# Kernel tuning notes

Hardware: AMD Instinct MI355X
Metric: run time of the kernel (lower is better)

The kernel has to match this reference:

```python
import math
import jax, jax.numpy as jnp
import numpy as np


def setup_inputs() -> dict:
    key = jax.random.key(0)
    k1, k2, k3 = jax.random.split(key, 3)
    B, T, D = 4, 2048, 2048
    x = jax.random.normal(k1, (B, T, D), dtype=jnp.float32)
    w_qkv = jax.random.normal(k2, (D, 3 * D), dtype=jnp.float32) * 0.02
    w_proj = jax.random.normal(k3, (D, D), dtype=jnp.float32) * 0.02
    b_proj = jnp.zeros((D,), dtype=jnp.float32)
    return {"x": x, "w_qkv": w_qkv, "w_proj": w_proj, "b_proj": b_proj, "n_head": 16}


def reference(x, w_qkv, w_proj, b_proj, n_head):
    B, T, D = x.shape
    N = n_head
    H = D // N
    qkv = x @ w_qkv                       # (B,T,3D)
    q, k, v = jnp.split(qkv, 3, axis=-1)  # each (B,T,D)
    # NOTE: original torch code does .view(B, n_head, T, H) directly on the
    # (B,T,D) tensor (a raw memory reinterpretation, not a head split+transpose).
    q = q.reshape(B, N, T, H)
    k = k.reshape(B, N, T, H)
    v = v.reshape(B, N, T, H)
    # full T x T score matrix, scaled by sqrt(D) (not sqrt(H)) as in the original
    a = jnp.einsum('bnih,bnjh->bnij', q, k) / math.sqrt(D)  # (B,N,T,T)
    a = jax.nn.softmax(a, axis=3)
    # torch.einsum('bntt,bnth->bnth', a, v): repeated 't' in first operand
    # takes the DIAGONAL of the attention matrix, then elementwise-scales v.
    diag = jnp.diagonal(a, axis1=2, axis2=3)  # (B,N,T)
    o = diag[..., None] * v                   # (B,N,T,H)
    o = jnp.transpose(o, (0, 2, 1, 3)).reshape(B, T, D)
    return o @ w_proj + b_proj
```

## Files before the change

kernel.cpp:

```cpp
#include <hip/hip_runtime.h>
#include <hip/hip_bf16.h>

typedef short bf16x8 __attribute__((ext_vector_type(8)));
typedef float f32x4 __attribute__((ext_vector_type(4)));

__device__ __forceinline__ unsigned short f2bf(float f) {
  union { float f; unsigned int u; } x; x.f = f;
  return (unsigned short)((x.u + 0x7fffu + ((x.u >> 16) & 1u)) >> 16);
}
__device__ __forceinline__ float bf2f(unsigned short u) {
  union { unsigned int u; float f; } x; x.u = ((unsigned int)u) << 16;
  return x.f;
}
__device__ __forceinline__ void gload_lds16(const void* g, void* l) {
  __builtin_amdgcn_global_load_lds((const __attribute__((address_space(1))) void*)g,
                                   (__attribute__((address_space(3))) void*)l, 16, 0, 0);
}

__global__ void cast_f32_bf16(const float* __restrict__ src, unsigned short* __restrict__ dst) {
  int i = blockIdx.x * blockDim.x + threadIdx.x;
  float4 v = reinterpret_cast<const float4*>(src)[i];
  ushort4 o;
  o.x = f2bf(v.x); o.y = f2bf(v.y); o.z = f2bf(v.z); o.w = f2bf(v.w);
  reinterpret_cast<ushort4*>(dst)[i] = o;
}

__global__ void transpose_cast(const float* __restrict__ src, unsigned short* __restrict__ dst,
                               int R, int C) {
  __shared__ float tile[32][33];
  int c0 = blockIdx.x * 32, r0 = blockIdx.y * 32;
  int tx = threadIdx.x, ty = threadIdx.y;
#pragma unroll
  for (int i = 0; i < 4; ++i)
    tile[ty + i * 8][tx] = src[(size_t)(r0 + ty + i * 8) * C + (c0 + tx)];
  __syncthreads();
#pragma unroll
  for (int i = 0; i < 4; ++i)
    dst[(size_t)(c0 + ty + i * 8) * R + (r0 + tx)] = f2bf(tile[tx][ty + i * 8]);
}

template <int EPI>
__global__ __launch_bounds__(512, 2)
void gemm256(const unsigned short* __restrict__ A, const unsigned short* __restrict__ Bt,
             unsigned short* __restrict__ Qo, unsigned short* __restrict__ Ko,
             unsigned short* __restrict__ Vo, float* __restrict__ Cf,
             const float* __restrict__ bias, int M, int N, int K) {
  extern __shared__ __align__(16) char lds[];
  const int tid = threadIdx.x;
  const int lane = tid & 63, wid = tid >> 6;
  const int wm = wid >> 2, wn = wid & 3;
  const int fr = lane & 15, fq = lane >> 4;

  const int nbn = N >> 8;
  const int cpx = gridDim.x >> 3;
  const int id = blockIdx.x;
  const int sw = (id & 7) * cpx + (id >> 3);
  const int bm = sw / nbn, bn = sw % nbn;
  const int row0 = bm << 8, col0 = bn << 8;

  const int NT = K >> 6;

  const int srow = tid >> 3;
  const int scol = ((tid & 7) ^ (srow & 7)) << 3;

  auto stage = [&](int j, int slot) {
    if (j < 4 * NT) {
      const int t = j >> 2, ht = j & 3;
      const int isB = (ht == 1 || ht == 2);
      const int h = (ht >= 2) ? 1 : 0;
      const unsigned short* base = isB ? Bt : A;
      const int grow = (isB ? col0 : row0) + h * 128 + srow;
      const unsigned short* src = base + (size_t)grow * K + t * 64 + scol;
      char* l0 = lds + slot * 16384 + tid * 16;
      gload_lds16(src, l0);
      gload_lds16(src + (size_t)64 * K, l0 + 8192);
    } else {
      char* l0 = lds + 7 * 16384 + tid * 16;
      gload_lds16(A + (tid << 3), l0);
      gload_lds16(A + (tid << 3), l0 + 8192);
    }
  };

  f32x4 acc[2][4][2][2] = {};

  stage(0, 0); stage(1, 1); stage(2, 2); stage(3, 3); stage(4, 4);
  asm volatile("s_waitcnt vmcnt(6)" ::: "memory");
  asm volatile("s_barrier" ::: "memory");

  int sA0 = 0, sB0 = 1, sB1 = 2, sA1 = 3, sst = 5;

  for (int k = 0; k < NT; ++k) {
    const int j0 = 4 * k + 5;
    bf16x8 a[4][2], b0[2][2], b1[2][2];

    {
      const char* Ab = lds + sA0 * 16384;
      const char* Bb = lds + sB0 * 16384;
#pragma unroll
      for (int i2 = 0; i2 < 4; ++i2)
#pragma unroll
        for (int ks = 0; ks < 2; ++ks) {
          const int byte = ((((wm * 4 + i2) * 16 + fr) * 128) + ks * 64 + fq * 16) ^ ((fr & 7) << 4);
          a[i2][ks] = *reinterpret_cast<const bf16x8*>(Ab + byte);
        }
#pragma unroll
      for (int j2 = 0; j2 < 2; ++j2)
#pragma unroll
        for (int ks = 0; ks < 2; ++ks) {
          const int byte = ((((wn * 2 + j2) * 16 + fr) * 128) + ks * 64 + fq * 16) ^ ((fr & 7) << 4);
          b0[j2][ks] = *reinterpret_cast<const bf16x8*>(Bb + byte);
        }
      stage(j0 + 0, sst); sst = (sst == 6) ? 0 : sst + 1;
      asm volatile("s_waitcnt vmcnt(6)" ::: "memory");
      asm volatile("s_barrier" ::: "memory");
      __builtin_amdgcn_s_setprio(1);
#pragma unroll
      for (int i2 = 0; i2 < 4; ++i2)
#pragma unroll
        for (int j2 = 0; j2 < 2; ++j2)
#pragma unroll
          for (int ks = 0; ks < 2; ++ks)
            acc[0][i2][0][j2] =
                __builtin_amdgcn_mfma_f32_16x16x32_bf16(a[i2][ks], b0[j2][ks], acc[0][i2][0][j2], 0, 0, 0);
      __builtin_amdgcn_s_setprio(0);
    }

    {
      const char* Bb = lds + sB1 * 16384;
#pragma unroll
      for (int j2 = 0; j2 < 2; ++j2)
#pragma unroll
        for (int ks = 0; ks < 2; ++ks) {
          const int byte = ((((wn * 2 + j2) * 16 + fr) * 128) + ks * 64 + fq * 16) ^ ((fr & 7) << 4);
          b1[j2][ks] = *reinterpret_cast<const bf16x8*>(Bb + byte);
        }
      stage(j0 + 1, sst); sst = (sst == 6) ? 0 : sst + 1;
      asm volatile("s_waitcnt vmcnt(6)" ::: "memory");
      asm volatile("s_barrier" ::: "memory");
      __builtin_amdgcn_s_setprio(1);
#pragma unroll
      for (int i2 = 0; i2 < 4; ++i2)
#pragma unroll
        for (int j2 = 0; j2 < 2; ++j2)
#pragma unroll
          for (int ks = 0; ks < 2; ++ks)
            acc[0][i2][1][j2] =
                __builtin_amdgcn_mfma_f32_16x16x32_bf16(a[i2][ks], b1[j2][ks], acc[0][i2][1][j2], 0, 0, 0);
      __builtin_amdgcn_s_setprio(0);
    }

    {
      const char* Ab = lds + sA1 * 16384;
#pragma unroll
      for (int i2 = 0; i2 < 4; ++i2)
#pragma unroll
        for (int ks = 0; ks < 2; ++ks) {
          const int byte = ((((wm * 4 + i2) * 16 + fr) * 128) + ks * 64 + fq * 16) ^ ((fr & 7) << 4);
          a[i2][ks] = *reinterpret_cast<const bf16x8*>(Ab + byte);
        }
      stage(j0 + 2, sst); sst = (sst == 6) ? 0 : sst + 1;
      asm volatile("s_waitcnt vmcnt(6)" ::: "memory");
      asm volatile("s_barrier" ::: "memory");
      __builtin_amdgcn_s_setprio(1);
#pragma unroll
      for (int i2 = 0; i2 < 4; ++i2)
#pragma unroll
        for (int j2 = 0; j2 < 2; ++j2)
#pragma unroll
          for (int ks = 0; ks < 2; ++ks)
            acc[1][i2][0][j2] =
                __builtin_amdgcn_mfma_f32_16x16x32_bf16(a[i2][ks], b0[j2][ks], acc[1][i2][0][j2], 0, 0, 0);
      __builtin_amdgcn_s_setprio(0);
    }

    {
      stage(j0 + 3, sst); sst = (sst == 6) ? 0 : sst + 1;
      asm volatile("s_waitcnt vmcnt(6)" ::: "memory");
      asm volatile("s_barrier" ::: "memory");
      __builtin_amdgcn_s_setprio(1);
#pragma unroll
      for (int i2 = 0; i2 < 4; ++i2)
#pragma unroll
        for (int j2 = 0; j2 < 2; ++j2)
#pragma unroll
          for (int ks = 0; ks < 2; ++ks)
            acc[1][i2][1][j2] =
                __builtin_amdgcn_mfma_f32_16x16x32_bf16(a[i2][ks], b1[j2][ks], acc[1][i2][1][j2], 0, 0, 0);
      __builtin_amdgcn_s_setprio(0);
    }

    sA0 += 4; if (sA0 >= 7) sA0 -= 7;
    sB0 += 4; if (sB0 >= 7) sB0 -= 7;
    sB1 += 4; if (sB1 >= 7) sB1 -= 7;
    sA1 += 4; if (sA1 >= 7) sA1 -= 7;
  }

  asm volatile("s_waitcnt vmcnt(0)" ::: "memory");

#pragma unroll
  for (int mh = 0; mh < 2; ++mh)
#pragma unroll
    for (int i2 = 0; i2 < 4; ++i2) {
      const int rbase = row0 + (mh * 8 + wm * 4 + i2) * 16 + fq * 4;
#pragma unroll
      for (int nh = 0; nh < 2; ++nh)
#pragma unroll
        for (int j2 = 0; j2 < 2; ++j2) {
          const int col = col0 + (nh * 8 + wn * 2 + j2) * 16 + fr;
#pragma unroll
          for (int r = 0; r < 4; ++r) {
            const float v = acc[mh][i2][nh][j2][r];
            const int row = rbase + r;
            if (EPI == 0) {
              const int seg = col >> 11, cc = col & 2047;
              unsigned short* dst = (seg == 0) ? Qo : (seg == 1 ? Ko : Vo);
              dst[(size_t)row * 2048 + cc] = f2bf(v);
            } else {
              Cf[(size_t)row * N + col] = v + bias[col];
            }
          }
        }
    }
}

__global__ __launch_bounds__(512, 2)
void attn_diag_ov(const unsigned short* __restrict__ Q, const unsigned short* __restrict__ K,
                  const unsigned short* __restrict__ V, unsigned short* __restrict__ OV) {
  __shared__ __align__(16) char ks[2][128 * 256];
  __shared__ float dlds[256];
  const int tid = threadIdx.x;
  const int lane = tid & 63, wid = tid >> 6;
  const int d = blockIdx.x;
  const int head = d & 63, tb = d >> 6;
  const int b = head >> 4, n = head & 15;
  const int t0 = tb << 8;
  const size_t hoff = (size_t)head << 18;
  const unsigned short* Qh = Q + hoff;
  const unsigned short* Kh = K + hoff;
  const unsigned short* Vh = V + hoff;

  const int fr = lane & 15, fq = lane >> 4;
  const int g4 = fq << 2;
  const int qrow0 = t0 + wid * 32;

  bf16x8 qf[2][4];
#pragma unroll
  for (int m = 0; m < 2; ++m)
#pragma unroll
    for (int kk = 0; kk < 4; ++kk)
      qf[m][kk] = *reinterpret_cast<const bf16x8*>(
          Qh + (size_t)(qrow0 + m * 16 + fr) * 128 + kk * 32 + fq * 8);

  auto stageK = [&](int jc, int s) {
    const char* ksrc = (const char*)(Kh + ((size_t)jc << 7));
#pragma unroll
    for (int i = 0; i < 4; ++i) {
      const int flat = i * 8192 + tid * 16;
      const int row = flat >> 8, c = (flat >> 4) & 15;
      const int sb = (row << 8) + ((c ^ (row & 15)) << 4);
      gload_lds16(ksrc + sb, &ks[s][0] + flat);
    }
  };

  float rsum[2][4] = {};
  float dnum[2][4] = {};
  const float scale = 0.02209708691207961f;

  stageK(0, 0);
  asm volatile("s_waitcnt vmcnt(0)" ::: "memory");
  asm volatile("s_barrier" ::: "memory");

  for (int t = 0; t < 16; ++t) {
    const int jc = t << 7;
    if (t < 15) stageK(jc + 128, (t + 1) & 1);
    const char* buf = &ks[t & 1][0];
#pragma unroll
    for (int jt = 0; jt < 8; ++jt) {
      bf16x8 bfrag[4];
#pragma unroll
      for (int kk = 0; kk < 4; ++kk) {
        const int row = jt * 16 + fr;
        const int s = kk * 4 + fq;
        bfrag[kk] = *reinterpret_cast<const bf16x8*>(buf + (row << 8) + ((s ^ (row & 15)) << 4));
      }
#pragma unroll
      for (int m = 0; m < 2; ++m) {
        f32x4 acc = {0.f, 0.f, 0.f, 0.f};
#pragma unroll
        for (int kk = 0; kk < 4; ++kk)
          acc = __builtin_amdgcn_mfma_f32_16x16x32_bf16(qf[m][kk], bfrag[kk], acc, 0, 0, 0);
        const int colj = jc + jt * 16 + fr;
        const int rowt = qrow0 + m * 16 + g4;
#pragma unroll
        for (int r = 0; r < 4; ++r) {
          const float e = __expf(acc[r] * scale);
          rsum[m][r] += e;
          if (colj == rowt + r) dnum[m][r] = e;
        }
      }
    }
    asm volatile("s_waitcnt vmcnt(0)" ::: "memory");
    asm volatile("s_barrier" ::: "memory");
  }

#pragma unroll
  for (int m = 0; m < 2; ++m)
#pragma unroll
    for (int r = 0; r < 4; ++r) {
#pragma unroll
      for (int s = 1; s < 16; s <<= 1) {
        rsum[m][r] += __shfl_xor(rsum[m][r], s, 64);
        dnum[m][r] += __shfl_xor(dnum[m][r], s, 64);
      }
      if (fr == 0) dlds[wid * 32 + m * 16 + g4 + r] = dnum[m][r] / rsum[m][r];
    }
  __syncthreads();

  const unsigned short* vsrc = Vh + ((size_t)t0 << 7);
  unsigned short* dst = OV + ((size_t)((b << 11) + t0)) * 2048 + (n << 7);
#pragma unroll
  for (int c = 0; c < 8; ++c) {
    const int flat = (c * 512 + tid) << 3;
    const int row = flat >> 7, col = flat & 127;
    bf16x8 v = *reinterpret_cast<const bf16x8*>(vsrc + flat);
    const float dd = dlds[row];
    bf16x8 o;
#pragma unroll
    for (int e = 0; e < 8; ++e)
      o[e] = (short)f2bf(bf2f((unsigned short)v[e]) * dd);
    *reinterpret_cast<bf16x8*>(dst + (size_t)row * 2048 + col) = o;
  }
}

extern "C" void kernel_launch(void* const* d_in, const int* in_sizes, int n_in,
                              void* d_out, int out_size, void* d_ws, size_t ws_size,
                              hipStream_t stream) {
  const float* x = (const float*)d_in[0];
  const float* w_qkv = (const float*)d_in[1];
  const float* w_proj = (const float*)d_in[2];
  const float* b_proj = (const float*)d_in[3];
  float* out = (float*)d_out;

  char* p = (char*)d_ws;
  unsigned short* Xb = (unsigned short*)p;     p += (size_t)8192 * 2048 * 2;
  unsigned short* WqkvT = (unsigned short*)p;  p += (size_t)6144 * 2048 * 2;
  unsigned short* WprojT = (unsigned short*)p; p += (size_t)2048 * 2048 * 2;
  unsigned short* Qb = (unsigned short*)p;     p += (size_t)8192 * 2048 * 2;
  unsigned short* Kb = (unsigned short*)p;     p += (size_t)8192 * 2048 * 2;
  unsigned short* Vb = (unsigned short*)p;     p += (size_t)8192 * 2048 * 2;
  unsigned short* OV = (unsigned short*)p;     p += (size_t)8192 * 2048 * 2;

  (void)hipFuncSetAttribute((const void*)gemm256<0>,
                            hipFuncAttributeMaxDynamicSharedMemorySize, 131072);
  (void)hipFuncSetAttribute((const void*)gemm256<1>,
                            hipFuncAttributeMaxDynamicSharedMemorySize, 131072);

  cast_f32_bf16<<<16384, 256, 0, stream>>>(x, Xb);
  transpose_cast<<<dim3(192, 64), dim3(32, 8), 0, stream>>>(w_qkv, WqkvT, 2048, 6144);
  transpose_cast<<<dim3(64, 64), dim3(32, 8), 0, stream>>>(w_proj, WprojT, 2048, 2048);

  gemm256<0><<<dim3(32 * 24), 512, 131072, stream>>>(Xb, WqkvT, Qb, Kb, Vb, nullptr, nullptr,
                                                     8192, 6144, 2048);
  attn_diag_ov<<<dim3(512), 512, 0, stream>>>(Qb, Kb, Vb, OV);
  gemm256<1><<<dim3(32 * 8), 512, 131072, stream>>>(OV, WprojT, nullptr, nullptr, nullptr, out,
                                                    b_proj, 8192, 2048, 2048);
}
```

Baseline: 375.7 us.

## Use 8-slot LDS ring with fixed slot mapping and drop two barriers per k-step

Moves the staging ring from 7 slots with rotating indices to 8 slots addressed as j&7, so each k-iteration reads from a fixed half chosen by k parity, and prefetch depth grows from 5 to 6 stages. With the deeper ring it removes the s_barrier after the first and third sub-steps, keeping two barriers per iteration, to cut synchronization stalls and slot-index arithmetic. It uses more LDS (128 KB), and the dropped barriers could open cross-wave hazards if the reuse distance is not large enough.

After: 353.0 us. 1.06x faster.

```diff
diff --git a/kernel.cpp b/kernel.cpp
--- a/kernel.cpp
+++ b/kernel.cpp
@@ -63,7 +63,8 @@
   const int srow = tid >> 3;
   const int scol = ((tid & 7) ^ (srow & 7)) << 3;
 
-  auto stage = [&](int j, int slot) {
+  auto stage = [&](int j) {
+    char* l0 = lds + (j & 7) * 16384 + tid * 16;
     if (j < 4 * NT) {
       const int t = j >> 2, ht = j & 3;
       const int isB = (ht == 1 || ht == 2);
@@ -71,11 +72,9 @@
       const unsigned short* base = isB ? Bt : A;
       const int grow = (isB ? col0 : row0) + h * 128 + srow;
       const unsigned short* src = base + (size_t)grow * K + t * 64 + scol;
-      char* l0 = lds + slot * 16384 + tid * 16;
       gload_lds16(src, l0);
       gload_lds16(src + (size_t)64 * K, l0 + 8192);
     } else {
-      char* l0 = lds + 7 * 16384 + tid * 16;
       gload_lds16(A + (tid << 3), l0);
       gload_lds16(A + (tid << 3), l0 + 8192);
     }
@@ -83,36 +82,36 @@
 
   f32x4 acc[2][4][2][2] = {};
 
-  stage(0, 0); stage(1, 1); stage(2, 2); stage(3, 3); stage(4, 4);
+  stage(0); stage(1); stage(2); stage(3); stage(4); stage(5);
   asm volatile("s_waitcnt vmcnt(6)" ::: "memory");
   asm volatile("s_barrier" ::: "memory");
 
-  int sA0 = 0, sB0 = 1, sB1 = 2, sA1 = 3, sst = 5;
-
   for (int k = 0; k < NT; ++k) {
-    const int j0 = 4 * k + 5;
+    const int j0 = 4 * k + 6;
+    const int sb = (k & 1) << 2;
+    const char* As0 = lds + (sb + 0) * 16384;
+    const char* Bs0 = lds + (sb + 1) * 16384;
+    const char* Bs1 = lds + (sb + 2) * 16384;
+    const char* As1 = lds + (sb + 3) * 16384;
     bf16x8 a[4][2], b0[2][2], b1[2][2];
 
     {
-      const char* Ab = lds + sA0 * 16384;
-      const char* Bb = lds + sB0 * 16384;
 #pragma unroll
       for (int i2 = 0; i2 < 4; ++i2)
 #pragma unroll
         for (int ks = 0; ks < 2; ++ks) {
           const int byte = ((((wm * 4 + i2) * 16 + fr) * 128) + ks * 64 + fq * 16) ^ ((fr & 7) << 4);
-          a[i2][ks] = *reinterpret_cast<const bf16x8*>(Ab + byte);
+          a[i2][ks] = *reinterpret_cast<const bf16x8*>(As0 + byte);
         }
 #pragma unroll
       for (int j2 = 0; j2 < 2; ++j2)
 #pragma unroll
         for (int ks = 0; ks < 2; ++ks) {
           const int byte = ((((wn * 2 + j2) * 16 + fr) * 128) + ks * 64 + fq * 16) ^ ((fr & 7) << 4);
-          b0[j2][ks] = *reinterpret_cast<const bf16x8*>(Bb + byte);
-        }
-      stage(j0 + 0, sst); sst = (sst == 6) ? 0 : sst + 1;
+          b0[j2][ks] = *reinterpret_cast<const bf16x8*>(Bs0 + byte);
+        }
+      stage(j0 + 0);
       asm volatile("s_waitcnt vmcnt(6)" ::: "memory");
-      asm volatile("s_barrier" ::: "memory");
       __builtin_amdgcn_s_setprio(1);
 #pragma unroll
       for (int i2 = 0; i2 < 4; ++i2)
@@ -126,15 +125,14 @@
     }
 
     {
-      const char* Bb = lds + sB1 * 16384;
 #pragma unroll
       for (int j2 = 0; j2 < 2; ++j2)
 #pragma unroll
         for (int ks = 0; ks < 2; ++ks) {
           const int byte = ((((wn * 2 + j2) * 16 + fr) * 128) + ks * 64 + fq * 16) ^ ((fr & 7) << 4);
-          b1[j2][ks] = *reinterpret_cast<const bf16x8*>(Bb + byte);
-        }
-      stage(j0 + 1, sst); sst = (sst == 6) ? 0 : sst + 1;
+          b1[j2][ks] = *reinterpret_cast<const bf16x8*>(Bs1 + byte);
+        }
+      stage(j0 + 1);
       asm volatile("s_waitcnt vmcnt(6)" ::: "memory");
       asm volatile("s_barrier" ::: "memory");
       __builtin_amdgcn_s_setprio(1);
@@ -150,17 +148,15 @@
     }
 
     {
-      const char* Ab = lds + sA1 * 16384;
 #pragma unroll
       for (int i2 = 0; i2 < 4; ++i2)
 #pragma unroll
         for (int ks = 0; ks < 2; ++ks) {
           const int byte = ((((wm * 4 + i2) * 16 + fr) * 128) + ks * 64 + fq * 16) ^ ((fr & 7) << 4);
-          a[i2][ks] = *reinterpret_cast<const bf16x8*>(Ab + byte);
-        }
-      stage(j0 + 2, sst); sst = (sst == 6) ? 0 : sst + 1;
+          a[i2][ks] = *reinterpret_cast<const bf16x8*>(As1 + byte);
+        }
+      stage(j0 + 2);
       asm volatile("s_waitcnt vmcnt(6)" ::: "memory");
-      asm volatile("s_barrier" ::: "memory");
       __builtin_amdgcn_s_setprio(1);
 #pragma unroll
       for (int i2 = 0; i2 < 4; ++i2)
@@ -174,7 +170,7 @@
     }
 
     {
-      stage(j0 + 3, sst); sst = (sst == 6) ? 0 : sst + 1;
+      stage(j0 + 3);
       asm volatile("s_waitcnt vmcnt(6)" ::: "memory");
       asm volatile("s_barrier" ::: "memory");
       __builtin_amdgcn_s_setprio(1);
@@ -188,11 +184,6 @@
                 __builtin_amdgcn_mfma_f32_16x16x32_bf16(a[i2][ks], b1[j2][ks], acc[1][i2][1][j2], 0, 0, 0);
       __builtin_amdgcn_s_setprio(0);
     }
-
-    sA0 += 4; if (sA0 >= 7) sA0 -= 7;
-    sB0 += 4; if (sB0 >= 7) sB0 -= 7;
-    sB1 += 4; if (sB1 >= 7) sB1 -= 7;
-    sA1 += 4; if (sA1 >= 7) sA1 -= 7;
   }
 
   asm volatile("s_waitcnt vmcnt(0)" ::: "memory");
```
